# Optimization experiments

Measured on AMD Instinct MI355X. Metric: run time of the kernel, lower is better.

The kernel has to match this reference:

```python
import jax, jax.numpy as jnp
import numpy as np

B0, C0, H0, W0 = 2, 64, 48, 48
BR, DI, NS, RK, K = 128, 128, 16, 4, 4
EPS = 1e-5


def _bn_relu(x, g, b):
    # eval-mode BatchNorm2d (running mean 0, var 1) followed by ReLU; x is NCHW
    return jax.nn.relu(x * (g / jnp.sqrt(1.0 + EPS))[None, :, None, None] + b[None, :, None, None])


def _c1(x, w):
    # 1x1 conv, w: (O, C, 1, 1)
    return jnp.einsum('bchw,oc->bohw', x, w[:, :, 0, 0])


def _avgpool(x, k, s, p):
    # torch AvgPool2d with count_include_pad=True -> divide by k*k
    y = jax.lax.reduce_window(x, 0.0, jax.lax.add, (1, 1, k, k), (1, 1, s, s), ((0, 0), (0, 0), (p, p), (p, p)))
    return y / float(k * k)


def _resize(x, h, w):
    # bilinear, align_corners=False (half-pixel), NCHW
    return jax.image.resize(x, (x.shape[0], x.shape[1], h, w), 'bilinear')


def _pappm(x, s0_g, s0_b, s0_w, s1_g, s1_b, s1_w, s2_g, s2_b, s2_w, s3_g, s3_b, s3_w, s4_g, s4_b, s4_w, comp_g, comp_b, comp_w, sc_g, sc_b, sc_w):
    h, w = x.shape[2], x.shape[3]
    x0 = _c1(_bn_relu(x, s0_g, s0_b), s0_w)
    y1 = _c1(_bn_relu(_avgpool(x, 3, 1, 1), s1_g, s1_b), s1_w) + x0  # stride-1 pool keeps size
    y2 = _resize(_c1(_bn_relu(_avgpool(x, 5, 2, 2), s2_g, s2_b), s2_w), h, w) + x0
    y3 = _resize(_c1(_bn_relu(_avgpool(x, 9, 4, 4), s3_g, s3_b), s3_w), h, w) + x0
    y4 = _c1(_bn_relu(x.mean((2, 3), keepdims=True), s4_g, s4_b), s4_w) + x0  # 1x1 -> broadcast
    cat = jnp.concatenate([x0, y1, y2, y3, y4], axis=1)  # (B, 5*BR, H, W)
    comp = jax.lax.conv_general_dilated(_bn_relu(cat, comp_g, comp_b), comp_w, (1, 1), ((1, 1), (1, 1)), dimension_numbers=('NCHW', 'OIHW', 'NCHW'))
    return comp + _c1(_bn_relu(x, sc_g, sc_b), sc_w)


def _ss2d(xin, in_proj_w, dw_w, dw_b, x_proj_w, dt_w, dt_b, A_logs, Ds, ln_g, ln_b, out_proj_w):
    # xin: (B, H, W, d_model)
    Bb, Hh, Ww, _ = xin.shape
    xz = xin @ in_proj_w.T                      # (B,H,W,2*DI)
    xc, z = jnp.split(xz, 2, axis=-1)
    xc = jnp.transpose(xc, (0, 3, 1, 2))        # (B,DI,H,W)
    xc = jax.lax.conv_general_dilated(xc, dw_w, (1, 1), ((1, 1), (1, 1)), dimension_numbers=('NCHW', 'OIHW', 'NCHW'), feature_group_count=DI)
    xc = jax.nn.silu(xc + dw_b[None, :, None, None])
    L = Hh * Ww
    x_hw = xc.reshape(Bb, DI, L)
    x_wh = jnp.transpose(xc, (0, 1, 3, 2)).reshape(Bb, DI, L)
    xs = jnp.stack([x_hw, x_wh, x_hw[:, :, ::-1], x_wh[:, :, ::-1]], axis=1)  # (B,K,DI,L)
    x_dbl = jnp.einsum('bkdl,kcd->bkcl', xs, x_proj_w)
    dts, Bm, Cm = jnp.split(x_dbl, [RK, RK + NS], axis=2)  # (B,K,RK,L),(B,K,NS,L),(B,K,NS,L)
    delta = jax.nn.softplus(jnp.einsum('bkrl,kdr->bkdl', dts, dt_w) + dt_b[None, :, :, None])  # (B,K,DI,L)
    A = -jnp.exp(A_logs).reshape(K, DI, NS)
    a = jnp.exp(delta[..., None] * A[None, :, :, None, :])                    # (B,K,DI,L,NS)
    bu = (delta * xs)[..., None] * jnp.transpose(Bm, (0, 1, 3, 2))[:, :, None]  # (B,K,DI,L,NS)

    def comb(e1, e2):
        a1, b1 = e1
        a2, b2 = e2
        return a2 * a1, a2 * b1 + b2

    _, hst = jax.lax.associative_scan(comb, (a, bu), axis=3)  # h_t = a_t*h_{t-1} + b_t
    y = jnp.einsum('bkdln,bknl->bkdl', hst, Cm) + xs * Ds.reshape(K, DI)[None, :, :, None]
    inv = y[:, 2:4][:, :, :, ::-1]
    y3 = jnp.transpose(y[:, 1].reshape(Bb, DI, Ww, Hh), (0, 1, 3, 2)).reshape(Bb, DI, L)
    y4 = jnp.transpose(inv[:, 1].reshape(Bb, DI, Ww, Hh), (0, 1, 3, 2)).reshape(Bb, DI, L)
    ys = jnp.transpose(y[:, 0] + inv[:, 0] + y3 + y4, (0, 2, 1)).reshape(Bb, Hh, Ww, DI)
    mu = ys.mean(-1, keepdims=True)
    var = jnp.mean((ys - mu) ** 2, -1, keepdims=True)
    yn = (ys - mu) / jnp.sqrt(var + EPS) * ln_g + ln_b
    return (yn * jax.nn.silu(z)) @ out_proj_w.T  # (B,H,W,d_model)


def setup_inputs():
    key = jax.random.key(0)
    ks = iter(jax.random.split(key, 32))
    nrm = lambda shp, s: jax.random.normal(next(ks), shp, jnp.float32) * s
    d = {}
    d['x'] = nrm((B0, C0, H0, W0), 1.0)
    for nm in ['s0', 's1', 's2', 's3', 's4']:
        d[nm + '_g'] = jnp.ones((C0,), jnp.float32)
        d[nm + '_b'] = jnp.zeros((C0,), jnp.float32)
        d[nm + '_w'] = nrm((BR, C0, 1, 1), (2.0 / C0) ** 0.5)
    d['comp_g'] = jnp.ones((5 * BR,), jnp.float32)
    d['comp_b'] = jnp.zeros((5 * BR,), jnp.float32)
    d['comp_w'] = nrm((C0, 5 * BR, 3, 3), (2.0 / (5 * BR * 9)) ** 0.5)
    d['sc_g'] = jnp.ones((C0,), jnp.float32)
    d['sc_b'] = jnp.zeros((C0,), jnp.float32)
    d['sc_w'] = nrm((C0, C0, 1, 1), (2.0 / C0) ** 0.5)
    d['in_proj_w'] = nrm((2 * DI, C0), C0 ** -0.5)
    d['dw_w'] = nrm((DI, 1, 3, 3), 0.3)
    d['dw_b'] = jnp.zeros((DI,), jnp.float32)
    d['x_proj_w'] = nrm((K, RK + 2 * NS, DI), DI ** -0.5)
    d['dt_w'] = nrm((K, DI, RK), RK ** -0.5)
    d['dt_b'] = jnp.log(jnp.expm1(jnp.asarray(0.01, jnp.float32))) * jnp.ones((K, DI), jnp.float32)
    d['A_logs'] = jnp.tile(jnp.log(jnp.arange(1, NS + 1, dtype=jnp.float32))[None], (K * DI, 1))
    d['Ds'] = jnp.ones((K * DI,), jnp.float32)
    d['ln_g'] = jnp.ones((DI,), jnp.float32)
    d['ln_b'] = jnp.zeros((DI,), jnp.float32)
    d['out_proj_w'] = nrm((C0, DI), DI ** -0.5)
    d['fc1_w'] = nrm((BR, C0, 1, 1), C0 ** -0.5)
    d['fc1_b'] = jnp.zeros((BR,), jnp.float32)
    d['fc2_w'] = nrm((C0, BR, 1, 1), BR ** -0.5)
    d['fc2_b'] = jnp.zeros((C0,), jnp.float32)
    return d


def reference(x, s0_g, s0_b, s0_w, s1_g, s1_b, s1_w, s2_g, s2_b, s2_w, s3_g, s3_b, s3_w, s4_g, s4_b, s4_w, comp_g, comp_b, comp_w, sc_g, sc_b, sc_w, in_proj_w, dw_w, dw_b, x_proj_w, dt_w, dt_b, A_logs, Ds, ln_g, ln_b, out_proj_w, fc1_w, fc1_b, fc2_w, fc2_b):
    p = _pappm(x, s0_g, s0_b, s0_w, s1_g, s1_b, s1_w, s2_g, s2_b, s2_w, s3_g, s3_b, s3_w, s4_g, s4_b, s4_w, comp_g, comp_b, comp_w, sc_g, sc_b, sc_w)
    a = _ss2d(jnp.transpose(p, (0, 2, 3, 1)), in_proj_w, dw_w, dw_b, x_proj_w, dt_w, dt_b, A_logs, Ds, ln_g, ln_b, out_proj_w)
    x1 = jnp.transpose(a, (0, 3, 1, 2))  # (B,C0,H,W)
    h1 = jax.nn.silu(_c1(x1, fc1_w) + fc1_b[None, :, None, None])
    return _c1(h1, fc2_w) + fc2_b[None, :, None, None] + x1
```

## Files before the change

### kernel.cpp

```cpp
#include <hip/hip_runtime.h>
#include <math.h>

constexpr int cB = 2, cC = 64, cH = 48, cW = 48, cL = 48 * 48;
constexpr int cBR = 128, cDI = 128, cNS = 16, cRK = 4, cK = 4;
constexpr float cEPS = 1e-5f;
constexpr int NCH = 32;
constexpr int CHL = cL / NCH;
constexpr int KTOT = 5824;

typedef unsigned short u16;
typedef unsigned int u32;
typedef short s16x8 __attribute__((ext_vector_type(8)));
typedef float f32x4 __attribute__((ext_vector_type(4)));

__device__ __forceinline__ float bnrelu(float v, float g, float b) {
    float y = v * (g * rsqrtf(1.0f + cEPS)) + b;
    return y > 0.f ? y : 0.f;
}
__device__ __forceinline__ float silu(float v) {
    return v / (1.f + expf(-v));
}
__device__ __forceinline__ u16 f2bf(float f) {
    u32 u = __float_as_uint(f);
    u = (u + 0x7fffu + ((u >> 16) & 1u)) >> 16;
    return (u16)u;
}
__device__ __forceinline__ s16x8 cvt8(const float* p) {
    s16x8 r;
#pragma unroll
    for (int i = 0; i < 8; i++) r[i] = (short)f2bf(p[i]);
    return r;
}
__device__ __forceinline__ float row_sum16(float v) {
    v += __int_as_float(__builtin_amdgcn_update_dpp(0, __float_as_int(v), 0xB1, 0xF, 0xF, true));
    v += __int_as_float(__builtin_amdgcn_update_dpp(0, __float_as_int(v), 0x4E, 0xF, 0xF, true));
    v += __int_as_float(__builtin_amdgcn_update_dpp(0, __float_as_int(v), 0x124, 0xF, 0xF, true));
    v += __int_as_float(__builtin_amdgcn_update_dpp(0, __float_as_int(v), 0x128, 0xF, 0xF, true));
    return v;
}

__global__ void __launch_bounds__(256) k_pools(const float* __restrict__ x, float* __restrict__ pool3,
                                               float* __restrict__ pool5, float* __restrict__ pool9,
                                               float* __restrict__ gmean) {
    __shared__ float sm[4];
    int blk = blockIdx.x;
    int t = threadIdx.x;
    if (blk < 1152) {
        int idx = blk * 256 + t;
        int w = idx % cW, h = (idx / cW) % cH, bc = idx / cL;
        const float* p = x + bc * cL;
        float s = 0.f;
        for (int dh = -1; dh <= 1; dh++) {
            int hh = h + dh; if (hh < 0 || hh >= cH) continue;
            for (int dw = -1; dw <= 1; dw++) {
                int ww = w + dw; if (ww < 0 || ww >= cW) continue;
                s += p[hh * cW + ww];
            }
        }
        pool3[idx] = s * (1.f / 9.f);
    } else if (blk < 1440) {
        int idx = (blk - 1152) * 256 + t;
        int w = idx % 24, h = (idx / 24) % 24, bc = idx / 576;
        const float* p = x + bc * cL;
        float s = 0.f;
        for (int kh = 0; kh < 5; kh++) {
            int hh = h * 2 - 2 + kh; if (hh < 0 || hh >= cH) continue;
            for (int kw = 0; kw < 5; kw++) {
                int ww = w * 2 - 2 + kw; if (ww < 0 || ww >= cW) continue;
                s += p[hh * cW + ww];
            }
        }
        pool5[idx] = s * (1.f / 25.f);
    } else if (blk < 1512) {
        int idx = (blk - 1440) * 256 + t;
        int w = idx % 12, h = (idx / 12) % 12, bc = idx / 144;
        const float* p = x + bc * cL;
        float s = 0.f;
        for (int kh = 0; kh < 9; kh++) {
            int hh = h * 4 - 4 + kh; if (hh < 0 || hh >= cH) continue;
            for (int kw = 0; kw < 9; kw++) {
                int ww = w * 4 - 4 + kw; if (ww < 0 || ww >= cW) continue;
                s += p[hh * cW + ww];
            }
        }
        pool9[idx] = s * (1.f / 81.f);
    } else {
        int bc = blk - 1512;
        const float* p = x + bc * cL;
        float s = 0.f;
        for (int i = t; i < cL; i += 256) s += p[i];
        for (int m = 32; m > 0; m >>= 1) s += __shfl_down(s, m);
        if ((t & 63) == 0) sm[t >> 6] = s;
        __syncthreads();
        if (t == 0) gmean[bc] = (sm[0] + sm[1] + sm[2] + sm[3]) * (1.f / cL);
    }
}

__global__ void __launch_bounds__(256) k_prep(const float* __restrict__ cw, const float* __restrict__ scw,
                                              const float* __restrict__ s0w, const float* __restrict__ s1w,
                                              const float* __restrict__ ipw, const float* __restrict__ xpw,
                                              u16* __restrict__ w8, u16* __restrict__ wcat,
                                              u16* __restrict__ ipk, u16* __restrict__ xpk) {
    int blk = blockIdx.x, t = threadIdx.x;
    if (blk < 1456) {
        int idx = blk * 256 + t;
        int o = idx / KTOT, kx = idx % KTOT;
        float v;
        if (kx < 5760) { int tap = kx / 640, ch = kx % 640; v = cw[(o * 640 + ch) * 9 + tap]; }
        else v = scw[o * 64 + (kx - 5760)];
        w8[(((size_t)(kx >> 3) * 64) + o) * 8 + (kx & 7)] = f2bf(v);
    } else if (blk < 1520) {
        int idx = (blk - 1456) * 256 + t;
        int g = idx >> 13, r = idx & 8191;
        int o = r >> 6, c = r & 63;
        float v = (g ? s1w : s0w)[r];
        int kt = c >> 5, q = (c >> 3) & 3, j = c & 7, nt = o >> 4, ln = o & 15;
        wcat[(size_t)((((g * 2 + kt) * 4 + q) * 8 + nt) * 16 + ln) * 8 + j] = f2bf(v);
    } else if (blk < 1584) {
        int idx = (blk - 1520) * 256 + t;
        int o = idx >> 6, c = idx & 63;
        int kt = c >> 5, q = (c >> 3) & 3, j = c & 7, nt = o >> 4, ln = o & 15;
        ipk[(size_t)(((kt * 4 + q) * 16 + nt) * 16 + ln) * 8 + j] = f2bf(ipw[idx]);
    } else {
        int idx = (blk - 1584) * 256 + t;
        int o = idx >> 7, d = idx & 127;
        int kt = d >> 5, q = (d >> 3) & 3, j = d & 7, nt = o >> 4, ln = o & 15;
        xpk[(size_t)(((kt * 4 + q) * 9 + nt) * 16 + ln) * 8 + j] = f2bf(xpw[idx]);
    }
}

__global__ void __launch_bounds__(128) k_c1all(const float* __restrict__ pool5, const float* __restrict__ pool9,
                                               const float* __restrict__ gm,
                                               const float* __restrict__ s2g, const float* __restrict__ s2b,
                                               const float* __restrict__ s2w,
                                               const float* __restrict__ s3g, const float* __restrict__ s3b,
                                               const float* __restrict__ s3w,
                                               const float* __restrict__ s4g, const float* __restrict__ s4b,
                                               const float* __restrict__ s4w,
                                               float* __restrict__ c2cl, float* __restrict__ c3cl,
                                               float* __restrict__ c4) {
    int pos = blockIdx.x;
    const float *in, *g, *bb, *w;
    float* outp;
    int HW, b, pp;
    if (pos < cB * 576) { b = pos / 576; pp = pos % 576; in = pool5; g = s2g; bb = s2b; w = s2w; HW = 576; outp = c2cl + ((size_t)b * 576 + pp) * 128; }
    else if (pos < cB * 576 + cB * 144) { int r = pos - cB * 576; b = r / 144; pp = r % 144; in = pool9; g = s3g; bb = s3b; w = s3w; HW = 144; outp = c3cl + ((size_t)b * 144 + pp) * 128; }
    else { b = pos - cB * 576 - cB * 144; pp = 0; in = gm; g = s4g; bb = s4b; w = s4w; HW = 1; outp = c4 + (size_t)b * 128; }
    __shared__ float v[64];
    int t = threadIdx.x;
    if (t < 64) v[t] = bnrelu(in[(b * 64 + t) * HW + pp], g[t], bb[t]);
    __syncthreads();
    float acc = 0.f;
    const float* wr = w + t * 64;
#pragma unroll 16
    for (int c = 0; c < 64; c++) acc += v[c] * wr[c];
    outp[t] = acc;
}

__global__ void __launch_bounds__(256) k_cat2(
    const float* __restrict__ x, const float* __restrict__ pool3, const float* __restrict__ c4,
    const float* __restrict__ s0g, const float* __restrict__ s0b,
    const float* __restrict__ s1g, const float* __restrict__ s1b,
    const float* __restrict__ scg, const float* __restrict__ scb,
    const float* __restrict__ cg, const float* __restrict__ cbb,
    const u16* __restrict__ wcat, const float* __restrict__ c2cl, const float* __restrict__ c3cl,
    u16* __restrict__ catbf, u16* __restrict__ xbf) {
    int blk = blockIdx.x;
    int b = blk / 144;
    int l0 = (blk % 144) * 16;
    int t = threadIdx.x;
    __shared__ float axv[16][68];
    __shared__ float ap3[16][68];
    __shared__ u16 axc[16][66];
    int pc = t >> 4, p = t & 15;
#pragma unroll
    for (int i = 0; i < 4; i++) {
        int c = i * 16 + pc;
        float xraw = x[(size_t)(b * 64 + c) * cL + l0 + p];
        float p3raw = pool3[(size_t)(b * 64 + c) * cL + l0 + p];
        axv[p][c] = bnrelu(xraw, s0g[c], s0b[c]);
        ap3[p][c] = bnrelu(p3raw, s1g[c], s1b[c]);
        axc[p][c] = f2bf(bnrelu(xraw, scg[c], scb[c]));
    }
    __syncthreads();
#pragma unroll
    for (int i = 0; i < 4; i++) {
        int idx = i * 256 + t;
        int pp = idx >> 6, cc = idx & 63;
        xbf[((size_t)b * cL + l0 + pp) * 64 + cc] = axc[pp][cc];
    }
    int wv = t >> 6, lane = t & 63, ln = lane & 15, q = lane >> 4;
    f32x4 ax[2] = {};
    f32x4 ay[2] = {};
#pragma unroll
    for (int kt = 0; kt < 2; kt++) {
        s16x8 a0 = cvt8(&axv[ln][kt * 32 + q * 8]);
        s16x8 a1 = cvt8(&ap3[ln][kt * 32 + q * 8]);
#pragma unroll
        for (int jj = 0; jj < 2; jj++) {
            int nt = wv * 2 + jj;
            s16x8 b0 = *(const s16x8*)(wcat + (size_t)((((0 * 2 + kt) * 4 + q) * 8 + nt) * 16 + ln) * 8);
            s16x8 b1 = *(const s16x8*)(wcat + (size_t)((((1 * 2 + kt) * 4 + q) * 8 + nt) * 16 + ln) * 8);
            ax[jj] = __builtin_amdgcn_mfma_f32_16x16x32_bf16(a0, b0, ax[jj], 0, 0, 0);
            ay[jj] = __builtin_amdgcn_mfma_f32_16x16x32_bf16(a1, b1, ay[jj], 0, 0, 0);
        }
    }
    int hrow = l0 / cW, w0g = l0 % cW;
    float sy2 = hrow * 0.5f - 0.25f;
    float fy2 = floorf(sy2); int iy2 = (int)fy2; float ay2 = sy2 - fy2;
    int y20 = min(max(iy2, 0), 23), y21 = min(max(iy2 + 1, 0), 23);
    float sy3 = hrow * 0.25f - 0.375f;
    float fy3 = floorf(sy3); int iy3 = (int)fy3; float ay3 = sy3 - fy3;
    int y30 = min(max(iy3, 0), 11), y31 = min(max(iy3 + 1, 0), 11);
    const float* c2b = c2cl + (size_t)b * 576 * 128;
    const float* c3b = c3cl + (size_t)b * 144 * 128;
#pragma unroll
    for (int r = 0; r < 4; r++) {
        int pp = q * 4 + r;
        int wq = w0g + pp;
        float sx2 = wq * 0.5f - 0.25f;
        float fx2 = floorf(sx2); int ix2 = (int)fx2; float ax2 = sx2 - fx2;
        int x20 = min(max(ix2, 0), 23), x21 = min(max(ix2 + 1, 0), 23);
        float sx3 = wq * 0.25f - 0.375f;
        float fx3 = floorf(sx3); int ix3 = (int)fx3; float ax3 = sx3 - fx3;
        int x30 = min(max(ix3, 0), 11), x31 = min(max(ix3 + 1, 0), 11);
#pragma unroll
        for (int jj = 0; jj < 2; jj++) {
            int ch = (wv * 2 + jj) * 16 + ln;
            float v00 = c2b[(y20 * 24 + x20) * 128 + ch], v01 = c2b[(y20 * 24 + x21) * 128 + ch];
            float v10 = c2b[(y21 * 24 + x20) * 128 + ch], v11 = c2b[(y21 * 24 + x21) * 128 + ch];
            float t0 = v00 + (v01 - v00) * ax2, t1 = v10 + (v11 - v10) * ax2;
            float u2v = t0 + (t1 - t0) * ay2;
            float w00 = c3b[(y30 * 12 + x30) * 128 + ch], w01 = c3b[(y30 * 12 + x31) * 128 + ch];
            float w10 = c3b[(y31 * 12 + x30) * 128 + ch], w11 = c3b[(y31 * 12 + x31) * 128 + ch];
            float s0_ = w00 + (w01 - w00) * ax3, s1_ = w10 + (w11 - w10) * ax3;
            float u3v = s0_ + (s1_ - s0_) * ay3;
            float x0 = ax[jj][r];
            float y1 = ay[jj][r] + x0;
            float y2 = x0 + u2v;
            float y3 = x0 + u3v;
            float y4 = x0 + c4[b * 128 + ch];
            u16* base = catbf + ((size_t)b * cL + l0 + pp) * 640;
            base[ch]       = f2bf(bnrelu(x0, cg[ch],       cbb[ch]));
            base[128 + ch] = f2bf(bnrelu(y1, cg[128 + ch], cbb[128 + ch]));
            base[256 + ch] = f2bf(bnrelu(y2, cg[256 + ch], cbb[256 + ch]));
            base[384 + ch] = f2bf(bnrelu(y3, cg[384 + ch], cbb[384 + ch]));
            base[512 + ch] = f2bf(bnrelu(y4, cg[512 + ch], cbb[512 + ch]));
        }
    }
}

__global__ void __launch_bounds__(512) k_compip(const u16* __restrict__ catbf,
                                                const u16* __restrict__ xbf,
                                                const u16* __restrict__ w8,
                                                const u16* __restrict__ ipk,
                                                float* __restrict__ xc, float* __restrict__ z) {
    int pix0 = blockIdx.x * 16;
    int b = pix0 / cL;
    int t = threadIdx.x;
    int wv = t >> 6, lane = t & 63, ln = lane & 15, q = lane >> 4;
    __shared__ float pl[8][16][68];
    __shared__ u16 pv16[16][72];
    int la = (pix0 + ln) - b * cL;
    int h = la / cW, w = la % cW;
    f32x4 acc[4] = {};
    int ks0 = wv * 23;
    int kcnt = (wv == 7) ? 21 : 23;
    for (int i = 0; i < kcnt; i++) {
        int ks = ks0 + i;
        s16x8 av;
        if (ks < 180) {
            int s = ks / 20;
            int cc = ks - s * 20;
            int s3 = s / 3;
            int kh = s3 - 1, kw = s - s3 * 3 - 1;
            int hh = h + kh, ww = w + kw;
            bool ok = (hh >= 0) && (hh < cH) && (ww >= 0) && (ww < cW);
            const u16* ap = catbf + (((size_t)b * cL + hh * cW + ww) * 640 + cc * 32 + q * 8);
            if (ok) av = *(const s16x8*)ap;
            else av = s16x8{0, 0, 0, 0, 0, 0, 0, 0};
        } else {
            int cc = ks - 180;
            av = *(const s16x8*)(xbf + (size_t)(pix0 + ln) * 64 + cc * 32 + q * 8);
        }
        const u16* wrow = w8 + ((size_t)ks * 4 + q) * 512;
#pragma unroll
        for (int j = 0; j < 4; j++) {
            s16x8 bv = *(const s16x8*)(wrow + (size_t)(j * 16 + ln) * 8);
            acc[j] = __builtin_amdgcn_mfma_f32_16x16x32_bf16(av, bv, acc[j], 0, 0, 0);
        }
    }
#pragma unroll
    for (int j = 0; j < 4; j++)
#pragma unroll
        for (int r = 0; r < 4; r++)
            pl[wv][q * 4 + r][j * 16 + ln] = acc[j][r];
    __syncthreads();
#pragma unroll
    for (int e = 0; e < 2; e++) {
        int id = e * 512 + t;
        int p = id >> 6, c = id & 63;
        float s = 0.f;
#pragma unroll
        for (int w2 = 0; w2 < 8; w2++) s += pl[w2][p][c];
        pv16[p][c] = f2bf(s);
    }
    __syncthreads();
    f32x4 a2[2] = {};
#pragma unroll
    for (int kt = 0; kt < 2; kt++) {
        s16x8 a = *(const s16x8*)(&pv16[ln][kt * 32 + q * 8]);
#pragma unroll
        for (int jn = 0; jn < 2; jn++) {
            int nt = wv * 2 + jn;
            s16x8 bfr = *(const s16x8*)(ipk + (size_t)(((kt * 4 + q) * 16 + nt) * 16 + ln) * 8);
            a2[jn] = __builtin_amdgcn_mfma_f32_16x16x32_bf16(a, bfr, a2[jn], 0, 0, 0);
        }
    }
#pragma unroll
    for (int jn = 0; jn < 2; jn++) {
        int o = (wv * 2 + jn) * 16 + ln;
#pragma unroll
        for (int r = 0; r < 4; r++) {
            int p = q * 4 + r;
            if (o < 128) xc[((size_t)pix0 + p) * 128 + o] = a2[jn][r];
            else         z[((size_t)pix0 + p) * 128 + (o - 128)] = a2[jn][r];
        }
    }
}

__global__ void k_dw(const float* __restrict__ xc, const float* __restrict__ dww,
                     const float* __restrict__ dwb, float* __restrict__ xca) {
    int idx = blockIdx.x * 256 + threadIdx.x;
    if (idx >= cB * cL * cDI) return;
    int d = idx & 127;
    int rest = idx >> 7;
    int l = rest % cL, b = rest / cL;
    int h = l / cW, w = l % cW;
    const float* base = xc + (size_t)b * cL * 128 + d;
    float acc = dwb[d];
    const float* kw = dww + d * 9;
    for (int i = 0; i < 3; i++) {
        int hh = h + i - 1; if (hh < 0 || hh >= cH) continue;
        for (int j = 0; j < 3; j++) {
            int ww = w + j - 1; if (ww < 0 || ww >= cW) continue;
            acc += base[(size_t)(hh * cW + ww) * 128] * kw[i * 3 + j];
        }
    }
    xca[idx] = silu(acc);
}

__global__ void __launch_bounds__(1024) k_xdbl4(const float* __restrict__ xca, const u16* __restrict__ xpk,
                                                const float* __restrict__ dtw, const float* __restrict__ dtb,
                                                float* __restrict__ bc, float* __restrict__ delta) {
    int blk = blockIdx.x;
    int b = blk / 144;
    int l0 = (blk % 144) * 16;
    int t = threadIdx.x;
    __shared__ float av[16][132];
    __shared__ float Dt[16][148];
#pragma unroll
    for (int i = 0; i < 2; i++) {
        int id = i * 1024 + t;
        int d = id & 127, p = id >> 7;
        av[p][d] = xca[((size_t)b * cL + l0 + p) * 128 + d];
    }
    __syncthreads();
    int wv = t >> 6, lane = t & 63, ln = lane & 15, q = lane >> 4;
    if (wv < 9) {
        int nt = wv;
        f32x4 acc = {};
#pragma unroll
        for (int kt = 0; kt < 4; kt++) {
            s16x8 a = cvt8(&av[ln][kt * 32 + q * 8]);
            s16x8 bfr = *(const s16x8*)(xpk + (size_t)(((kt * 4 + q) * 9 + nt) * 16 + ln) * 8);
            acc = __builtin_amdgcn_mfma_f32_16x16x32_bf16(a, bfr, acc, 0, 0, 0);
        }
#pragma unroll
        for (int r = 0; r < 4; r++)
            Dt[q * 4 + r][nt * 16 + ln] = acc[r];
    }
    __syncthreads();
#pragma unroll
    for (int i = 0; i < 2; i++) {
        int id = i * 1024 + t;
        int cc = id & 31, kk = (id >> 5) & 3, p = id >> 7;
        bc[((size_t)(b * 4 + kk) * cL + l0 + p) * 32 + cc] = Dt[p][kk * 36 + 4 + cc];
    }
    {
        int d = t & 127;
        int kk = (t >> 7) & 3;
        int p0 = t >> 9;
        const float* wd = dtw + (size_t)(kk * 128 + d) * 4;
        float w0 = wd[0], w1 = wd[1], w2 = wd[2], w3 = wd[3];
        float bb = dtb[kk * 128 + d];
        float* dout = delta + ((size_t)(b * 4 + kk) * cL + l0) * 128 + d;
#pragma unroll
        for (int i = 0; i < 8; i++) {
            int p = p0 + i * 2;
            float pre = bb + w0 * Dt[p][kk * 36] + w1 * Dt[p][kk * 36 + 1]
                      + w2 * Dt[p][kk * 36 + 2] + w3 * Dt[p][kk * 36 + 3];
            float dl = pre > 20.f ? pre : log1pf(expf(pre));
            dout[(size_t)p * 128] = dl;
        }
    }
}

__device__ __forceinline__ int xs_index(int k, int l) {
    int lp = (k & 2) ? (cL - 1 - l) : l;
    if (k & 1) { int w = lp / cH, h = lp % cH; return h * cW + w; }
    return lp;
}

__global__ void __launch_bounds__(256) k_scan1(const float* __restrict__ delta, const float* __restrict__ xca,
                                               const float* __restrict__ bc, const float* __restrict__ Alogs,
                                               float* __restrict__ Pend, float* __restrict__ hend) {
    int blk = blockIdx.x;
    int c = blk & 31;
    if (c == NCH - 1) return;
    int g = blk >> 5;
    int dgq = g & 7, bk = g >> 3;
    int k = bk & 3, b = bk >> 2;
    int t = threadIdx.x;
    int n = t & 15;
    int d = dgq * 16 + (t >> 4);
    float A = -expf(Alogs[(k * 128 + d) * 16 + n]);
    const float* dp = delta + (size_t)bk * cL * 128 + d;
    const float* xp = xca + (size_t)b * cL * 128 + d;
    const float* bp = bc + (size_t)bk * cL * 32 + n;
    int off = xs_index(k, c * CHL);
    int step = (k == 0) ? 1 : (k == 1) ? cW : (k == 2) ? -1 : -cW;
    float P = 1.f, h = 0.f;
#pragma unroll 4
    for (int i = 0; i < CHL; i++) {
        float dl = dp[(size_t)off * 128];
        float a = expf(dl * A);
        h = a * h + dl * xp[(size_t)off * 128] * bp[(size_t)off * 32];
        P *= a;
        off += step;
        if (off >= cL) off -= (cL - 1);
        else if (off < 0) off += (cL - 1);
    }
    Pend[(size_t)blk * 256 + t] = P;
    hend[(size_t)blk * 256 + t] = h;
}

__global__ void __launch_bounds__(256) k_scan2(const float* __restrict__ Pend, float* __restrict__ hend) {
    int id = blockIdx.x * 256 + threadIdx.x;
    int t = id & 255;
    int g = id >> 8;
    float h = 0.f;
    for (int c = 0; c < NCH; c++) {
        size_t idx = ((size_t)g * NCH + c) * 256 + t;
        float tmp = hend[idx];
        float Pv = Pend[idx];
        hend[idx] = h;
        h = Pv * h + tmp;
    }
}

__global__ void __launch_bounds__(256) k_scan3(const float* __restrict__ delta, const float* __restrict__ xca,
                                               const float* __restrict__ bc, const float* __restrict__ Alogs,
                                               const float* __restrict__ Dsv, const float* __restrict__ hinb,
                                               float* __restrict__ y) {
    int blk = blockIdx.x;
    int c = blk & 31;
    int g = blk >> 5;
    int dgq = g & 7, bk = g >> 3;
    int k = bk & 3, b = bk >> 2;
    int t = threadIdx.x;
    int n = t & 15;
    int d = dgq * 16 + (t >> 4);
    float A = -expf(Alogs[(k * 128 + d) * 16 + n]);
    float Dsd = Dsv[k * 128 + d];
    const float* dp = delta + (size_t)bk * cL * 128 + d;
    const float* xp = xca + (size_t)b * cL * 128 + d;
    const float* bp = bc + (size_t)bk * cL * 32 + n;
    const float* cp = bc + (size_t)bk * cL * 32 + 16 + n;
    float* yb = y + (size_t)bk * cL * 128 + d;
    int off = xs_index(k, c * CHL);
    int step = (k == 0) ? 1 : (k == 1) ? cW : (k == 2) ? -1 : -cW;
    float h = hinb[(size_t)blk * 256 + t];
#pragma unroll 2
    for (int i = 0; i < CHL; i++) {
        float dl = dp[(size_t)off * 128];
        float xv = xp[(size_t)off * 128];
        float a = expf(dl * A);
        h = a * h + dl * xv * bp[(size_t)off * 32];
        float contrib = row_sum16(h * cp[(size_t)off * 32]);
        if (n == 0) yb[(size_t)off * 128] = contrib + xv * Dsd;
        off += step;
        if (off >= cL) off -= (cL - 1);
        else if (off < 0) off += (cL - 1);
    }
}

__global__ void __launch_bounds__(256) k_tail(const float* __restrict__ y, const float* __restrict__ z,
                                              const float* __restrict__ lng, const float* __restrict__ lnb,
                                              const float* __restrict__ opw,
                                              const float* __restrict__ f1w, const float* __restrict__ f1b,
                                              const float* __restrict__ f2w, const float* __restrict__ f2b,
                                              float* __restrict__ out) {
    int blk = blockIdx.x;
    int b = blk / 288;
    int l0 = (blk % 288) * 8;
    int t = threadIdx.x;
    __shared__ float v[8][132];
    __shared__ float x1s[8][68];
    __shared__ float h1s[8][132];
    __shared__ float mus[8], rss[8];
    const float* yb = y + (size_t)b * 4 * cL * 128;
#pragma unroll
    for (int i = 0; i < 4; i++) {
        int id = i * 256 + t;
        int d = id & 127, p = id >> 7;
        size_t base = (size_t)(l0 + p) * 128 + d;
        v[p][d] = yb[base] + yb[(size_t)cL * 128 + base] + yb[(size_t)2 * cL * 128 + base] + yb[(size_t)3 * cL * 128 + base];
    }
    __syncthreads();
    if (t < 128) {
        int p = t >> 4, c8 = (t & 15) * 8;
        float s = 0.f;
#pragma unroll
        for (int j = 0; j < 8; j++) s += v[p][c8 + j];
        s = row_sum16(s);
        float mu = s * (1.f / 128.f);
        float s2 = 0.f;
#pragma unroll
        for (int j = 0; j < 8; j++) { float dv = v[p][c8 + j] - mu; s2 += dv * dv; }
        s2 = row_sum16(s2);
        if ((t & 15) == 0) { mus[p] = mu; rss[p] = rsqrtf(s2 * (1.f / 128.f) + cEPS); }
    }
    __syncthreads();
#pragma unroll
    for (int i = 0; i < 4; i++) {
        int id = i * 256 + t;
        int d = id & 127, p = id >> 7;
        float zz = z[((size_t)b * cL + l0 + p) * 128 + d];
        v[p][d] = ((v[p][d] - mus[p]) * rss[p] * lng[d] + lnb[d]) * silu(zz);
    }
    __syncthreads();
#pragma unroll
    for (int i = 0; i < 2; i++) {
        int id = i * 256 + t;
        int p = id & 7, o = id >> 3;
        const float* wr = opw + o * 128;
        float acc = 0.f;
#pragma unroll 16
        for (int d2 = 0; d2 < 128; d2++) acc += v[p][d2] * wr[d2];
        x1s[p][o] = acc;
    }
    __syncthreads();
#pragma unroll
    for (int i = 0; i < 4; i++) {
        int id = i * 256 + t;
        int p = id & 7, j = id >> 3;
        const float* wr = f1w + j * 64;
        float acc = f1b[j];
#pragma unroll 16
        for (int c = 0; c < 64; c++) acc += x1s[p][c] * wr[c];
        h1s[p][j] = silu(acc);
    }
    __syncthreads();
#pragma unroll
    for (int i = 0; i < 2; i++) {
        int id = i * 256 + t;
        int p = id & 7, o = id >> 3;
        const float* wr = f2w + o * 128;
        float acc = f2b[o];
#pragma unroll 16
        for (int j = 0; j < 128; j++) acc += h1s[p][j] * wr[j];
        out[((size_t)b * 64 + o) * cL + l0 + p] = acc + x1s[p][o];
    }
}

extern "C" void kernel_launch(void* const* d_in, const int* in_sizes, int n_in,
                              void* d_out, int out_size, void* d_ws, size_t ws_size,
                              hipStream_t stream) {
    (void)in_sizes; (void)n_in; (void)out_size; (void)ws_size;
    const float* x    = (const float*)d_in[0];
    const float* s0g  = (const float*)d_in[1];
    const float* s0b  = (const float*)d_in[2];
    const float* s0w  = (const float*)d_in[3];
    const float* s1g  = (const float*)d_in[4];
    const float* s1b  = (const float*)d_in[5];
    const float* s1w  = (const float*)d_in[6];
    const float* s2g  = (const float*)d_in[7];
    const float* s2b  = (const float*)d_in[8];
    const float* s2w  = (const float*)d_in[9];
    const float* s3g  = (const float*)d_in[10];
    const float* s3b  = (const float*)d_in[11];
    const float* s3w  = (const float*)d_in[12];
    const float* s4g  = (const float*)d_in[13];
    const float* s4b  = (const float*)d_in[14];
    const float* s4w  = (const float*)d_in[15];
    const float* cg   = (const float*)d_in[16];
    const float* cbb  = (const float*)d_in[17];
    const float* cw   = (const float*)d_in[18];
    const float* scg  = (const float*)d_in[19];
    const float* scb  = (const float*)d_in[20];
    const float* scw  = (const float*)d_in[21];
    const float* ipw  = (const float*)d_in[22];
    const float* dww  = (const float*)d_in[23];
    const float* dwb  = (const float*)d_in[24];
    const float* xpw  = (const float*)d_in[25];
    const float* dtw  = (const float*)d_in[26];
    const float* dtb  = (const float*)d_in[27];
    const float* Alog = (const float*)d_in[28];
    const float* Dsv  = (const float*)d_in[29];
    const float* lng  = (const float*)d_in[30];
    const float* lnb  = (const float*)d_in[31];
    const float* opw  = (const float*)d_in[32];
    const float* f1w  = (const float*)d_in[33];
    const float* f1b  = (const float*)d_in[34];
    const float* f2w  = (const float*)d_in[35];
    const float* f2b  = (const float*)d_in[36];
    float* out = (float*)d_out;

    float* ws = (float*)d_ws;
    size_t off = 0;
    float* pool3  = ws + off; off += 294912;
    float* pool5  = ws + off; off += 73728;
    float* pool9  = ws + off; off += 18432;
    float* gmean  = ws + off; off += 128;
    float* c2cl   = ws + off; off += 147456;
    float* c3cl   = ws + off; off += 36864;
    float* c4     = ws + off; off += 256;
    u16*   catbf  = (u16*)(ws + off); off += 1474560;
    u16*   xbf    = (u16*)(ws + off); off += 147456;
    u16*   w8     = (u16*)(ws + off); off += 186368;
    u16*   wcat   = (u16*)(ws + off); off += 8192;
    u16*   ipk    = (u16*)(ws + off); off += 8192;
    float* xc     = ws + off; off += 589824;
    u16*   xpk    = (u16*)(ws + off); off += 9216;
    float* xca    = ws + off; off += 589824;
    float* zbuf   = ws + off; off += 589824;
    float* bcbuf  = ws + off; off += 589824;
    float* Pend   = ws + off; off += 524288;
    float* ybuf   = ws + off; off += 2359296;
    off += 294912;
    float* delta  = ws + 0;
    float* hend   = xc;

    k_pools<<<1640, 256, 0, stream>>>(x, pool3, pool5, pool9, gmean);
    k_prep<<<1656, 256, 0, stream>>>(cw, scw, s0w, s1w, ipw, xpw, w8, wcat, ipk, xpk);
    k_c1all<<<cB * 576 + cB * 144 + cB, 128, 0, stream>>>(pool5, pool9, gmean, s2g, s2b, s2w,
                                                          s3g, s3b, s3w, s4g, s4b, s4w, c2cl, c3cl, c4);
    k_cat2<<<cB * 144, 256, 0, stream>>>(x, pool3, c4, s0g, s0b, s1g, s1b, scg, scb, cg, cbb,
                                         wcat, c2cl, c3cl, catbf, xbf);
    k_compip<<<cB * cL / 16, 512, 0, stream>>>(catbf, xbf, w8, ipk, xc, zbuf);
    k_dw<<<(cB * cL * 128 + 255) / 256, 256, 0, stream>>>(xc, dww, dwb, xca);
    k_xdbl4<<<cB * 144, 1024, 0, stream>>>(xca, xpk, dtw, dtb, bcbuf, delta);
    k_scan1<<<64 * NCH, 256, 0, stream>>>(delta, xca, bcbuf, Alog, Pend, hend);
    k_scan2<<<64, 256, 0, stream>>>(Pend, hend);
    k_scan3<<<64 * NCH, 256, 0, stream>>>(delta, xca, bcbuf, Alog, Dsv, hend, ybuf);
    k_tail<<<cB * 288, 256, 0, stream>>>(ybuf, zbuf, lng, lnb, opw, f1w, f1b, f2w, f2b, out);
}
```

Baseline: 302.8 us.

## Merge pool and prep kernels, vectorize depthwise conv, widen cat2 and shrink tail blocks

Merges the pooling and weight-prep kernels into one launch, which now also transposes the depthwise weights into a tap-major layout. The depthwise conv is vectorized to process four channels per thread with float4 loads. k_cat2 moves to 512 threads so each wave handles one output tile, and k_tail now covers 4 positions per block instead of 8, doubling the grid. Together these aim to cut launch overhead, memory transactions and per-thread serial work, at the cost of more blocks and a slightly larger workspace.

```diff
diff --git a/kernel.cpp b/kernel.cpp
--- a/kernel.cpp
+++ b/kernel.cpp
@@ -39,9 +39,16 @@
     return v;
 }
 
-__global__ void __launch_bounds__(256) k_pools(const float* __restrict__ x, float* __restrict__ pool3,
-                                               float* __restrict__ pool5, float* __restrict__ pool9,
-                                               float* __restrict__ gmean) {
+__global__ void __launch_bounds__(256) k_pp(const float* __restrict__ x, float* __restrict__ pool3,
+                                            float* __restrict__ pool5, float* __restrict__ pool9,
+                                            float* __restrict__ gmean,
+                                            const float* __restrict__ cw, const float* __restrict__ scw,
+                                            const float* __restrict__ s0w, const float* __restrict__ s1w,
+                                            const float* __restrict__ ipw, const float* __restrict__ xpw,
+                                            const float* __restrict__ dww,
+                                            u16* __restrict__ w8, u16* __restrict__ wcat,
+                                            u16* __restrict__ ipk, u16* __restrict__ xpk,
+                                            float* __restrict__ dwk) {
     __shared__ float sm[4];
     int blk = blockIdx.x;
     int t = threadIdx.x;
@@ -84,7 +91,7 @@
             }
         }
         pool9[idx] = s * (1.f / 81.f);
-    } else {
+    } else if (blk < 1640) {
         int bc = blk - 1512;
         const float* p = x + bc * cL;
         float s = 0.f;
@@ -93,39 +100,36 @@
         if ((t & 63) == 0) sm[t >> 6] = s;
         __syncthreads();
         if (t == 0) gmean[bc] = (sm[0] + sm[1] + sm[2] + sm[3]) * (1.f / cL);
-    }
-}
-
-__global__ void __launch_bounds__(256) k_prep(const float* __restrict__ cw, const float* __restrict__ scw,
-                                              const float* __restrict__ s0w, const float* __restrict__ s1w,
-                                              const float* __restrict__ ipw, const float* __restrict__ xpw,
-                                              u16* __restrict__ w8, u16* __restrict__ wcat,
-                                              u16* __restrict__ ipk, u16* __restrict__ xpk) {
-    int blk = blockIdx.x, t = threadIdx.x;
-    if (blk < 1456) {
-        int idx = blk * 256 + t;
+    } else if (blk < 3096) {
+        int idx = (blk - 1640) * 256 + t;
         int o = idx / KTOT, kx = idx % KTOT;
         float v;
         if (kx < 5760) { int tap = kx / 640, ch = kx % 640; v = cw[(o * 640 + ch) * 9 + tap]; }
         else v = scw[o * 64 + (kx - 5760)];
         w8[(((size_t)(kx >> 3) * 64) + o) * 8 + (kx & 7)] = f2bf(v);
-    } else if (blk < 1520) {
-        int idx = (blk - 1456) * 256 + t;
+    } else if (blk < 3160) {
+        int idx = (blk - 3096) * 256 + t;
         int g = idx >> 13, r = idx & 8191;
         int o = r >> 6, c = r & 63;
         float v = (g ? s1w : s0w)[r];
         int kt = c >> 5, q = (c >> 3) & 3, j = c & 7, nt = o >> 4, ln = o & 15;
         wcat[(size_t)((((g * 2 + kt) * 4 + q) * 8 + nt) * 16 + ln) * 8 + j] = f2bf(v);
-    } else if (blk < 1584) {
-        int idx = (blk - 1520) * 256 + t;
+    } else if (blk < 3224) {
+        int idx = (blk - 3160) * 256 + t;
         int o = idx >> 6, c = idx & 63;
         int kt = c >> 5, q = (c >> 3) & 3, j = c & 7, nt = o >> 4, ln = o & 15;
         ipk[(size_t)(((kt * 4 + q) * 16 + nt) * 16 + ln) * 8 + j] = f2bf(ipw[idx]);
-    } else {
-        int idx = (blk - 1584) * 256 + t;
+    } else if (blk < 3296) {
+        int idx = (blk - 3224) * 256 + t;
         int o = idx >> 7, d = idx & 127;
         int kt = d >> 5, q = (d >> 3) & 3, j = d & 7, nt = o >> 4, ln = o & 15;
         xpk[(size_t)(((kt * 4 + q) * 9 + nt) * 16 + ln) * 8 + j] = f2bf(xpw[idx]);
+    } else {
+        int idx = (blk - 3296) * 256 + t;
+        if (idx < 1152) {
+            int tap = idx >> 7, ch = idx & 127;
+            dwk[idx] = dww[ch * 9 + tap];
+        }
     }
 }
 
@@ -157,7 +161,7 @@
     outp[t] = acc;
 }
 
-__global__ void __launch_bounds__(256) k_cat2(
+__global__ void __launch_bounds__(512) k_cat2(
     const float* __restrict__ x, const float* __restrict__ pool3, const float* __restrict__ c4,
     const float* __restrict__ s0g, const float* __restrict__ s0b,
     const float* __restrict__ s1g, const float* __restrict__ s1b,
@@ -172,10 +176,10 @@
     __shared__ float axv[16][68];
     __shared__ float ap3[16][68];
     __shared__ u16 axc[16][66];
-    int pc = t >> 4, p = t & 15;
-#pragma unroll
-    for (int i = 0; i < 4; i++) {
-        int c = i * 16 + pc;
+    int p = t & 15, c0 = t >> 4;
+#pragma unroll
+    for (int i = 0; i < 2; i++) {
+        int c = i * 32 + c0;
         float xraw = x[(size_t)(b * 64 + c) * cL + l0 + p];
         float p3raw = pool3[(size_t)(b * 64 + c) * cL + l0 + p];
         axv[p][c] = bnrelu(xraw, s0g[c], s0b[c]);
@@ -184,26 +188,22 @@
     }
     __syncthreads();
 #pragma unroll
-    for (int i = 0; i < 4; i++) {
-        int idx = i * 256 + t;
+    for (int i = 0; i < 2; i++) {
+        int idx = i * 512 + t;
         int pp = idx >> 6, cc = idx & 63;
         xbf[((size_t)b * cL + l0 + pp) * 64 + cc] = axc[pp][cc];
     }
     int wv = t >> 6, lane = t & 63, ln = lane & 15, q = lane >> 4;
-    f32x4 ax[2] = {};
-    f32x4 ay[2] = {};
+    f32x4 ax = {};
+    f32x4 ay = {};
 #pragma unroll
     for (int kt = 0; kt < 2; kt++) {
         s16x8 a0 = cvt8(&axv[ln][kt * 32 + q * 8]);
         s16x8 a1 = cvt8(&ap3[ln][kt * 32 + q * 8]);
-#pragma unroll
-        for (int jj = 0; jj < 2; jj++) {
-            int nt = wv * 2 + jj;
-            s16x8 b0 = *(const s16x8*)(wcat + (size_t)((((0 * 2 + kt) * 4 + q) * 8 + nt) * 16 + ln) * 8);
-            s16x8 b1 = *(const s16x8*)(wcat + (size_t)((((1 * 2 + kt) * 4 + q) * 8 + nt) * 16 + ln) * 8);
-            ax[jj] = __builtin_amdgcn_mfma_f32_16x16x32_bf16(a0, b0, ax[jj], 0, 0, 0);
-            ay[jj] = __builtin_amdgcn_mfma_f32_16x16x32_bf16(a1, b1, ay[jj], 0, 0, 0);
-        }
+        s16x8 b0 = *(const s16x8*)(wcat + (size_t)((((0 * 2 + kt) * 4 + q) * 8 + wv) * 16 + ln) * 8);
+        s16x8 b1 = *(const s16x8*)(wcat + (size_t)((((1 * 2 + kt) * 4 + q) * 8 + wv) * 16 + ln) * 8);
+        ax = __builtin_amdgcn_mfma_f32_16x16x32_bf16(a0, b0, ax, 0, 0, 0);
+        ay = __builtin_amdgcn_mfma_f32_16x16x32_bf16(a1, b1, ay, 0, 0, 0);
     }
     int hrow = l0 / cW, w0g = l0 % cW;
     float sy2 = hrow * 0.5f - 0.25f;
@@ -214,6 +214,8 @@
     int y30 = min(max(iy3, 0), 11), y31 = min(max(iy3 + 1, 0), 11);
     const float* c2b = c2cl + (size_t)b * 576 * 128;
     const float* c3b = c3cl + (size_t)b * 144 * 128;
+    int ch = wv * 16 + ln;
+    float c4v = c4[b * 128 + ch];
 #pragma unroll
     for (int r = 0; r < 4; r++) {
         int pp = q * 4 + r;
@@ -224,29 +226,25 @@
         float sx3 = wq * 0.25f - 0.375f;
         float fx3 = floorf(sx3); int ix3 = (int)fx3; float ax3 = sx3 - fx3;
         int x30 = min(max(ix3, 0), 11), x31 = min(max(ix3 + 1, 0), 11);
-#pragma unroll
-        for (int jj = 0; jj < 2; jj++) {
-            int ch = (wv * 2 + jj) * 16 + ln;
-            float v00 = c2b[(y20 * 24 + x20) * 128 + ch], v01 = c2b[(y20 * 24 + x21) * 128 + ch];
-            float v10 = c2b[(y21 * 24 + x20) * 128 + ch], v11 = c2b[(y21 * 24 + x21) * 128 + ch];
-            float t0 = v00 + (v01 - v00) * ax2, t1 = v10 + (v11 - v10) * ax2;
-            float u2v = t0 + (t1 - t0) * ay2;
-            float w00 = c3b[(y30 * 12 + x30) * 128 + ch], w01 = c3b[(y30 * 12 + x31) * 128 + ch];
-            float w10 = c3b[(y31 * 12 + x30) * 128 + ch], w11 = c3b[(y31 * 12 + x31) * 128 + ch];
-            float s0_ = w00 + (w01 - w00) * ax3, s1_ = w10 + (w11 - w10) * ax3;
-            float u3v = s0_ + (s1_ - s0_) * ay3;
-            float x0 = ax[jj][r];
-            float y1 = ay[jj][r] + x0;
-            float y2 = x0 + u2v;
-            float y3 = x0 + u3v;
-            float y4 = x0 + c4[b * 128 + ch];
-            u16* base = catbf + ((size_t)b * cL + l0 + pp) * 640;
-            base[ch]       = f2bf(bnrelu(x0, cg[ch],       cbb[ch]));
-            base[128 + ch] = f2bf(bnrelu(y1, cg[128 + ch], cbb[128 + ch]));
-            base[256 + ch] = f2bf(bnrelu(y2, cg[256 + ch], cbb[256 + ch]));
-            base[384 + ch] = f2bf(bnrelu(y3, cg[384 + ch], cbb[384 + ch]));
-            base[512 + ch] = f2bf(bnrelu(y4, cg[512 + ch], cbb[512 + ch]));
-        }
+        float v00 = c2b[(y20 * 24 + x20) * 128 + ch], v01 = c2b[(y20 * 24 + x21) * 128 + ch];
+        float v10 = c2b[(y21 * 24 + x20) * 128 + ch], v11 = c2b[(y21 * 24 + x21) * 128 + ch];
+        float t0 = v00 + (v01 - v00) * ax2, t1 = v10 + (v11 - v10) * ax2;
+        float u2v = t0 + (t1 - t0) * ay2;
+        float w00 = c3b[(y30 * 12 + x30) * 128 + ch], w01 = c3b[(y30 * 12 + x31) * 128 + ch];
+        float w10 = c3b[(y31 * 12 + x30) * 128 + ch], w11 = c3b[(y31 * 12 + x31) * 128 + ch];
+        float s0_ = w00 + (w01 - w00) * ax3, s1_ = w10 + (w11 - w10) * ax3;
+        float u3v = s0_ + (s1_ - s0_) * ay3;
+        float x0 = ax[r];
+        float y1 = ay[r] + x0;
+        float y2 = x0 + u2v;
+        float y3 = x0 + u3v;
+        float y4 = x0 + c4v;
+        u16* base = catbf + ((size_t)b * cL + l0 + pp) * 640;
+        base[ch]       = f2bf(bnrelu(x0, cg[ch],       cbb[ch]));
+        base[128 + ch] = f2bf(bnrelu(y1, cg[128 + ch], cbb[128 + ch]));
+        base[256 + ch] = f2bf(bnrelu(y2, cg[256 + ch], cbb[256 + ch]));
+        base[384 + ch] = f2bf(bnrelu(y3, cg[384 + ch], cbb[384 + ch]));
+        base[512 + ch] = f2bf(bnrelu(y4, cg[512 + ch], cbb[512 + ch]));
     }
 }
 
@@ -329,25 +327,31 @@
     }
 }
 
-__global__ void k_dw(const float* __restrict__ xc, const float* __restrict__ dww,
-                     const float* __restrict__ dwb, float* __restrict__ xca) {
+__global__ void __launch_bounds__(256) k_dw(const float* __restrict__ xc, const float* __restrict__ dwk,
+                                            const float* __restrict__ dwb, float* __restrict__ xca) {
     int idx = blockIdx.x * 256 + threadIdx.x;
-    if (idx >= cB * cL * cDI) return;
-    int d = idx & 127;
-    int rest = idx >> 7;
+    int d4 = idx & 31;
+    int rest = idx >> 5;
     int l = rest % cL, b = rest / cL;
     int h = l / cW, w = l % cW;
-    const float* base = xc + (size_t)b * cL * 128 + d;
-    float acc = dwb[d];
-    const float* kw = dww + d * 9;
+    const f32x4* xb = (const f32x4*)xc + (size_t)b * cL * 32;
+    const f32x4* kb = (const f32x4*)dwk;
+    f32x4 acc = ((const f32x4*)dwb)[d4];
+#pragma unroll
     for (int i = 0; i < 3; i++) {
         int hh = h + i - 1; if (hh < 0 || hh >= cH) continue;
+#pragma unroll
         for (int j = 0; j < 3; j++) {
             int ww = w + j - 1; if (ww < 0 || ww >= cW) continue;
-            acc += base[(size_t)(hh * cW + ww) * 128] * kw[i * 3 + j];
-        }
-    }
-    xca[idx] = silu(acc);
+            f32x4 v = xb[(size_t)(hh * cW + ww) * 32 + d4];
+            f32x4 kv = kb[(i * 3 + j) * 32 + d4];
+            acc += v * kv;
+        }
+    }
+    f32x4 r;
+#pragma unroll
+    for (int c = 0; c < 4; c++) r[c] = silu(acc[c]);
+    ((f32x4*)xca)[idx] = r;
 }
 
 __global__ void __launch_bounds__(1024) k_xdbl4(const float* __restrict__ xca, const u16* __restrict__ xpk,
@@ -502,23 +506,23 @@
                                               const float* __restrict__ f2w, const float* __restrict__ f2b,
                                               float* __restrict__ out) {
     int blk = blockIdx.x;
-    int b = blk / 288;
-    int l0 = (blk % 288) * 8;
-    int t = threadIdx.x;
-    __shared__ float v[8][132];
-    __shared__ float x1s[8][68];
-    __shared__ float h1s[8][132];
-    __shared__ float mus[8], rss[8];
+    int b = blk / 576;
+    int l0 = (blk % 576) * 4;
+    int t = threadIdx.x;
+    __shared__ float v[4][132];
+    __shared__ float x1s[4][68];
+    __shared__ float h1s[4][132];
+    __shared__ float mus[4], rss[4];
     const float* yb = y + (size_t)b * 4 * cL * 128;
 #pragma unroll
-    for (int i = 0; i < 4; i++) {
+    for (int i = 0; i < 2; i++) {
         int id = i * 256 + t;
         int d = id & 127, p = id >> 7;
         size_t base = (size_t)(l0 + p) * 128 + d;
         v[p][d] = yb[base] + yb[(size_t)cL * 128 + base] + yb[(size_t)2 * cL * 128 + base] + yb[(size_t)3 * cL * 128 + base];
     }
     __syncthreads();
-    if (t < 128) {
+    if (t < 64) {
         int p = t >> 4, c8 = (t & 15) * 8;
         float s = 0.f;
 #pragma unroll
@@ -533,17 +537,15 @@
     }
     __syncthreads();
 #pragma unroll
-    for (int i = 0; i < 4; i++) {
+    for (int i = 0; i < 2; i++) {
         int id = i * 256 + t;
         int d = id & 127, p = id >> 7;
         float zz = z[((size_t)b * cL + l0 + p) * 128 + d];
         v[p][d] = ((v[p][d] - mus[p]) * rss[p] * lng[d] + lnb[d]) * silu(zz);
     }
     __syncthreads();
-#pragma unroll
-    for (int i = 0; i < 2; i++) {
-        int id = i * 256 + t;
-        int p = id & 7, o = id >> 3;
+    {
+        int p = t & 3, o = t >> 2;
         const float* wr = opw + o * 128;
         float acc = 0.f;
 #pragma unroll 16
@@ -552,9 +554,9 @@
     }
     __syncthreads();
 #pragma unroll
-    for (int i = 0; i < 4; i++) {
+    for (int i = 0; i < 2; i++) {
         int id = i * 256 + t;
-        int p = id & 7, j = id >> 3;
+        int p = id & 3, j = id >> 2;
         const float* wr = f1w + j * 64;
         float acc = f1b[j];
 #pragma unroll 16
@@ -562,10 +564,8 @@
         h1s[p][j] = silu(acc);
     }
     __syncthreads();
-#pragma unroll
-    for (int i = 0; i < 2; i++) {
-        int id = i * 256 + t;
-        int p = id & 7, o = id >> 3;
+    {
+        int p = t & 3, o = t >> 2;
         const float* wr = f2w + o * 128;
         float acc = f2b[o];
 #pragma unroll 16
@@ -633,6 +633,7 @@
     u16*   ipk    = (u16*)(ws + off); off += 8192;
     float* xc     = ws + off; off += 589824;
     u16*   xpk    = (u16*)(ws + off); off += 9216;
+    float* dwk    = ws + off; off += 1280;
     float* xca    = ws + off; off += 589824;
     float* zbuf   = ws + off; off += 589824;
     float* bcbuf  = ws + off; off += 589824;
@@ -642,17 +643,18 @@
     float* delta  = ws + 0;
     float* hend   = xc;
 
-    k_pools<<<1640, 256, 0, stream>>>(x, pool3, pool5, pool9, gmean);
-    k_prep<<<1656, 256, 0, stream>>>(cw, scw, s0w, s1w, ipw, xpw, w8, wcat, ipk, xpk);
+    k_pp<<<3301, 256, 0, stream>>>(x, pool3, pool5, pool9, gmean,
+                                   cw, scw, s0w, s1w, ipw, xpw, dww,
+                                   w8, wcat, ipk, xpk, dwk);
     k_c1all<<<cB * 576 + cB * 144 + cB, 128, 0, stream>>>(pool5, pool9, gmean, s2g, s2b, s2w,
                                                           s3g, s3b, s3w, s4g, s4b, s4w, c2cl, c3cl, c4);
-    k_cat2<<<cB * 144, 256, 0, stream>>>(x, pool3, c4, s0g, s0b, s1g, s1b, scg, scb, cg, cbb,
+    k_cat2<<<cB * 144, 512, 0, stream>>>(x, pool3, c4, s0g, s0b, s1g, s1b, scg, scb, cg, cbb,
                                          wcat, c2cl, c3cl, catbf, xbf);
     k_compip<<<cB * cL / 16, 512, 0, stream>>>(catbf, xbf, w8, ipk, xc, zbuf);
-    k_dw<<<(cB * cL * 128 + 255) / 256, 256, 0, stream>>>(xc, dww, dwb, xca);
+    k_dw<<<cB * cL * 128 / 4 / 256, 256, 0, stream>>>(xc, dwk, dwb, xca);
     k_xdbl4<<<cB * 144, 1024, 0, stream>>>(xca, xpk, dtw, dtb, bcbuf, delta);
     k_scan1<<<64 * NCH, 256, 0, stream>>>(delta, xca, bcbuf, Alog, Pend, hend);
     k_scan2<<<64, 256, 0, stream>>>(Pend, hend);
     k_scan3<<<64 * NCH, 256, 0, stream>>>(delta, xca, bcbuf, Alog, Dsv, hend, ybuf);
-    k_tail<<<cB * 288, 256, 0, stream>>>(ybuf, zbuf, lng, lnb, opw, f1w, f1b, f2w, f2b, out);
-}
+    k_tail<<<cB * 576, 256, 0, stream>>>(ybuf, zbuf, lng, lnb, opw, f1w, f1b, f2w, f2b, out);
+}
```

After: 288.1 us. 4.9% less time.
